# Performance work log

Measured on AMD Instinct MI355X. Metric: run time of the kernel, lower is better.

## Reference

```python
import jax, jax.numpy as jnp
import numpy as np

D_MODEL = 1024
N_HEADS = 16
HEAD_DIM = D_MODEL // N_HEADS  # 64


def setup_inputs() -> dict:
    key = jax.random.key(0)
    k1, k2, k3 = jax.random.split(key, 3)
    x = jax.random.normal(k1, (2, 2048, D_MODEL), dtype=jnp.float32)
    # nn.Linear(d, 3d, bias=False): store transposed so y = x @ W
    w_qkv = jax.random.normal(k2, (D_MODEL, 3 * D_MODEL), dtype=jnp.float32) * (D_MODEL ** -0.5)
    w_proj = jax.random.normal(k3, (D_MODEL, D_MODEL), dtype=jnp.float32) * (D_MODEL ** -0.5)
    return {"x": x, "w_qkv": w_qkv, "w_proj": w_proj}


def reference(x, w_qkv, w_proj):
    b, n, _ = x.shape
    qkv = x @ w_qkv  # [b, n, 3*d_model]
    # einops 'b n (h d qkv) -> qkv b h n d': qkv axis is innermost of the split
    qkv = qkv.reshape(b, n, N_HEADS, HEAD_DIM, 3)
    q = jnp.moveaxis(qkv[..., 0], 1, 2)  # [b, h, n, d]
    k = jnp.moveaxis(qkv[..., 1], 1, 2)
    v = jnp.moveaxis(qkv[..., 2], 1, 2)
    scale = HEAD_DIM ** -0.5
    scores = jnp.einsum('bhqd,bhkd->bhqk', q, k) * scale  # [b, h, n, n]
    causal = jnp.tril(jnp.ones((n, n), dtype=bool))
    scores = jnp.where(causal[None, None], scores, -jnp.inf)
    attn = jax.nn.softmax(scores, axis=-1)
    out = jnp.einsum('bhqk,bhkd->bhqd', attn, v)  # [b, h, n, d]
    out = jnp.moveaxis(out, 1, 2).reshape(b, n, D_MODEL)  # 'b h n d -> b n (h d)'
    return out @ w_proj
```

## Files before the change

kernel.cpp:

```cpp
#include <hip/hip_runtime.h>
#include <cstdint>
#include <cstddef>

#define D_MODEL 1024
#define N_HEADS 16
#define HEAD_DIM 64
#define SEQ 2048
#define BATCH 2

typedef __attribute__((ext_vector_type(8))) short bf16x8;
typedef __attribute__((ext_vector_type(4))) float f32x4;

__device__ inline unsigned short f2bf(float f) {
    union { float f; unsigned u; } v; v.f = f;
    unsigned r = v.u + 0x7fffu + ((v.u >> 16) & 1u);
    return (unsigned short)(r >> 16);
}

__device__ __forceinline__ unsigned cvtpk_bf16(float lo, float hi) {
    unsigned r;
    asm("v_cvt_pk_bf16_f32 %0, %1, %2" : "=v"(r) : "v"(lo), "v"(hi));
    return r;
}
__device__ __forceinline__ unsigned short f2bf_hw(float f) {
    return (unsigned short)cvtpk_bf16(f, 0.f);
}

__device__ __forceinline__ void gload_lds16(const unsigned short* g, unsigned short* l) {
    __builtin_amdgcn_global_load_lds(
        (const __attribute__((address_space(1))) unsigned int*)g,
        (__attribute__((address_space(3))) unsigned int*)l, 16, 0, 0);
}

#define WAITCNT_VM4 0x0F74
#define WAITCNT_VM0 0x0F70

__global__ __launch_bounds__(256) void fused_convert_kernel(
    const float* __restrict__ X, unsigned short* __restrict__ Xb,
    const float* __restrict__ Wq, unsigned short* __restrict__ Wqt,
    const float* __restrict__ Wp, unsigned short* __restrict__ Wpt)
{
    const int blk = blockIdx.x;
    const int tid = threadIdx.x;
    __shared__ float t[32][33];

    if (blk < 2048) {
        const int idx = blk * 256 + tid;
        const float4* src = (const float4*)X;
        float4 v0 = src[idx * 2], v1 = src[idx * 2 + 1];
        uint4 o;
        o.x = cvtpk_bf16(v0.x, v0.y);
        o.y = cvtpk_bf16(v0.z, v0.w);
        o.z = cvtpk_bf16(v1.x, v1.y);
        o.w = cvtpk_bf16(v1.z, v1.w);
        ((uint4*)Xb)[idx] = o;
    } else if (blk < 5120) {
        const int bb = blk - 2048;
        const int c0 = (bb % 96) * 32, r0 = (bb / 96) * 32;
        const int a = tid & 31, b = tid >> 5;
#pragma unroll
        for (int i = 0; i < 32; i += 8)
            t[b + i][a] = Wq[(size_t)(r0 + b + i) * (3 * D_MODEL) + c0 + a];
        __syncthreads();
#pragma unroll
        for (int i = 0; i < 32; i += 8) {
            const int c = c0 + b + i;
            const int which = c % 3;
            const int np = which * 1024 + c / 3;
            const float s = (which == 0) ? 0.125f : 1.0f;
            Wqt[(size_t)np * D_MODEL + r0 + a] = f2bf_hw(t[a][b + i] * s);
        }
    } else {
        const int bb = blk - 5120;
        const int c0 = (bb % 32) * 32, r0 = (bb / 32) * 32;
        const int a = tid & 31, b = tid >> 5;
#pragma unroll
        for (int i = 0; i < 32; i += 8)
            t[b + i][a] = Wp[(size_t)(r0 + b + i) * D_MODEL + c0 + a];
        __syncthreads();
#pragma unroll
        for (int i = 0; i < 32; i += 8)
            Wpt[(size_t)(c0 + b + i) * D_MODEL + r0 + a] = f2bf_hw(t[a][b + i]);
    }
}

#define GEMM_PIPE3_BODY(A_, B_, KBASE, NITER, BX_, BY_)                        \
    const int tid = threadIdx.x;                                               \
    const int w = tid >> 6, lane = tid & 63;                                   \
    const int l15 = lane & 15, quad = lane >> 4;                               \
    const int wr = w >> 1, wc = w & 1;                                         \
    const int row0 = (BY_) * 128, col0 = (BX_) * 128;                          \
    __shared__ unsigned short As[3][4096];                                     \
    __shared__ unsigned short Bs[3][4096];                                     \
    const f32x4 zero4 = {0.f, 0.f, 0.f, 0.f};                                  \
    f32x4 acc[4][4];                                                           \
    _Pragma("unroll") for (int i = 0; i < 4; i++)                              \
        _Pragma("unroll") for (int j = 0; j < 4; j++) acc[i][j] = zero4;       \
    auto stage_ = [&](int sb_, int kt_) {                                      \
        const int k0 = (KBASE) + kt_ * 32 + quad * 8;                          \
        _Pragma("unroll") for (int i = 0; i < 2; i++) {                        \
            const int f = w * 2 + i;                                           \
            gload_lds16((A_) + (size_t)(row0 + f * 16 + l15) * D_MODEL + k0,   \
                        &As[sb_][f * 512 + lane * 8]);                         \
            gload_lds16((B_) + (size_t)(col0 + f * 16 + l15) * D_MODEL + k0,   \
                        &Bs[sb_][f * 512 + lane * 8]);                         \
        }                                                                      \
    };                                                                         \
    stage_(0, 0);                                                              \
    stage_(1, 1);                                                              \
    int sb = 0;                                                                \
    for (int kt = 0; kt < (NITER); kt++) {                                     \
        if (kt < (NITER) - 1) {                                                \
            __builtin_amdgcn_s_waitcnt(WAITCNT_VM4);                           \
            __builtin_amdgcn_s_barrier();                                      \
            if (kt + 2 < (NITER)) stage_((sb + 2 > 2) ? sb - 1 : sb + 2, kt + 2); \
        } else {                                                               \
            __builtin_amdgcn_s_waitcnt(WAITCNT_VM0);                           \
            __builtin_amdgcn_s_barrier();                                      \
        }                                                                      \
        bf16x8 af[4], bfr[4];                                                  \
        _Pragma("unroll") for (int i = 0; i < 4; i++)                          \
            af[i] = *(const bf16x8*)&As[sb][(wr * 4 + i) * 512 + lane * 8];    \
        _Pragma("unroll") for (int j = 0; j < 4; j++)                          \
            bfr[j] = *(const bf16x8*)&Bs[sb][(wc * 4 + j) * 512 + lane * 8];   \
        __builtin_amdgcn_s_setprio(1);                                         \
        _Pragma("unroll") for (int i = 0; i < 4; i++)                          \
            _Pragma("unroll") for (int j = 0; j < 4; j++)                      \
                acc[i][j] = __builtin_amdgcn_mfma_f32_16x16x32_bf16(           \
                    af[i], bfr[j], acc[i][j], 0, 0, 0);                        \
        __builtin_amdgcn_s_setprio(0);                                         \
        sb = (sb == 2) ? 0 : sb + 1;                                           \
    }

__global__ __launch_bounds__(256) void gemm_qkv_mfma(
    const unsigned short* __restrict__ A, const unsigned short* __restrict__ B,
    unsigned short* __restrict__ Q, unsigned short* __restrict__ Kq,
    unsigned short* __restrict__ Vt)
{
    const int lin = blockIdx.x + 24 * blockIdx.y;
    const int xcd = lin & 7, t = lin >> 3;
    const int bx = (xcd & 1) * 12 + t % 12;
    const int by = (xcd >> 1) * 8 + t / 12;
    GEMM_PIPE3_BODY(A, B, 0, 32, bx, by)
    const int nbase = col0 + wc * 64;
    const int which = nbase >> 10;
    if (which < 2) {
        unsigned short* const dst = (which == 0) ? Q : Kq;
#pragma unroll
        for (int i = 0; i < 4; i++) {
            const int rowb = row0 + wr * 64 + i * 16 + quad * 4;
            const int bb = rowb >> 11, n = rowb & (SEQ - 1);
#pragma unroll
            for (int rp = 0; rp < 2; rp++) {
#pragma unroll
                for (int j = 0; j < 4; j++) {
                    const unsigned u = cvtpk_bf16(acc[i][j][2 * rp], acc[i][j][2 * rp + 1]);
                    const int idx = (nbase + j * 16 + l15) & 1023;
                    const int h = idx >> 6, dd = idx & 63;
                    unsigned short* p =
                        dst + (((size_t)(bb * N_HEADS + h)) * SEQ + n + 2 * rp) * HEAD_DIM + dd;
                    p[0] = (unsigned short)u;
                    p[HEAD_DIM] = (unsigned short)(u >> 16);
                }
            }
        }
    } else {
#pragma unroll
        for (int i = 0; i < 4; i++) {
            const int rowb = row0 + wr * 64 + i * 16 + quad * 4;
            const int bb = rowb >> 11, n = rowb & (SEQ - 1);
#pragma unroll
            for (int rp = 0; rp < 2; rp++) {
#pragma unroll
                for (int j = 0; j < 4; j++) {
                    const unsigned u = cvtpk_bf16(acc[i][j][2 * rp], acc[i][j][2 * rp + 1]);
                    const int idx = (nbase + j * 16 + l15) & 1023;
                    *(unsigned*)&Vt[((size_t)(bb * N_HEADS + (idx >> 6)) * HEAD_DIM
                                     + (idx & 63)) * SEQ + n + 2 * rp] = u;
                }
            }
        }
    }
}

__global__ __launch_bounds__(256) void gemm_proj_splitk(
    const unsigned short* __restrict__ A, const unsigned short* __restrict__ B,
    float* __restrict__ P)
{
    const int lin = blockIdx.x + 8 * blockIdx.y;
    const int xcd = lin & 7, t = lin >> 3;
    const int bx = (xcd & 1) * 4 + t % 4;
    const int by = (xcd >> 1) * 8 + t / 4;
    const int kbase = blockIdx.z * 512;
    GEMM_PIPE3_BODY(A, B, kbase, 16, bx, by)
    float* const dst = P + (size_t)blockIdx.z * (4096ull * 1024ull);
#pragma unroll
    for (int i = 0; i < 4; i++) {
#pragma unroll
        for (int r = 0; r < 4; r++) {
            const int row = row0 + wr * 64 + i * 16 + quad * 4 + r;
#pragma unroll
            for (int j = 0; j < 4; j++) {
                const int c = col0 + wc * 64 + j * 16 + l15;
                dst[(size_t)row * D_MODEL + c] = acc[i][j][r];
            }
        }
    }
}

__global__ __launch_bounds__(256) void add_out_kernel(
    const float* __restrict__ P, float* __restrict__ out)
{
    const float4* p0 = (const float4*)P;
    const float4* p1 = (const float4*)(P + 4096ull * 1024ull);
    float4* o = (float4*)out;
    const int base = (blockIdx.x * 256 + threadIdx.x) * 4;
#pragma unroll
    for (int j = 0; j < 4; j++) {
        float4 a = p0[base + j], b = p1[base + j];
        float4 r = {a.x + b.x, a.y + b.y, a.z + b.z, a.w + b.w};
        o[base + j] = r;
    }
}

__global__ __launch_bounds__(256) void flash_attn_kernel(
    const unsigned short* __restrict__ Q,
    const unsigned short* __restrict__ K,
    const unsigned short* __restrict__ Vt,
    unsigned short* __restrict__ O)
{
    const int idx = blockIdx.x;
    const int bh = idx & 31;
    const int qt2 = idx >> 5;
    const int hi = qt2 >> 3, lo = qt2 & 7;
    const int qt = (hi == 0) ? lo : (hi == 1) ? 31 - lo : (hi == 2) ? lo + 8 : 23 - lo;

    const int tid = threadIdx.x;
    const int w = tid >> 6, lane = tid & 63;
    const int l15 = lane & 15, quad = lane >> 4;

    __shared__ unsigned short Ks[2][4096];
    __shared__ unsigned short Vs[2][4096];
    __shared__ unsigned short Ps[4][1024];

    bf16x8 qf[2];
    {
        const unsigned short* qrow =
            Q + ((size_t)bh * SEQ + qt * 64 + w * 16 + l15) * HEAD_DIM;
        qf[0] = *(const bf16x8*)(qrow + quad * 8);
        qf[1] = *(const bf16x8*)(qrow + 32 + quad * 8);
    }

    const f32x4 zero4 = {0.f, 0.f, 0.f, 0.f};
    f32x4 o_acc[4] = {zero4, zero4, zero4, zero4};
    float m_i = -1e30f, l_i = 0.f;

    auto stage = [&](int bf, int kt_t) {
        const int key0 = kt_t * 64;
#pragma unroll
        for (int i = 0; i < 2; i++) {
            const int f = w * 2 + i;
            const int ct = f >> 1, kh = f & 1;
            gload_lds16(K + ((size_t)bh * SEQ + key0 + ct * 16 + l15) * HEAD_DIM
                          + kh * 32 + quad * 8,
                        &Ks[bf][f * 512 + lane * 8]);
            gload_lds16(Vt + ((size_t)bh * HEAD_DIM + ct * 16 + l15) * SEQ
                           + key0 + kh * 32 + quad * 8,
                        &Vs[bf][f * 512 + lane * 8]);
        }
    };

    stage(0, 0);
    int buf = 0;

    const int qg = qt * 64 + w * 16 + l15;

    for (int kt = 0; kt <= qt; kt++) {
        __syncthreads();
        if (kt < qt) stage(buf ^ 1, kt + 1);

        f32x4 st[4] = {zero4, zero4, zero4, zero4};
        __builtin_amdgcn_s_setprio(1);
#pragma unroll
        for (int kh = 0; kh < 2; kh++) {
#pragma unroll
            for (int ct = 0; ct < 4; ct++) {
                bf16x8 kf = *(const bf16x8*)&Ks[buf][(ct * 2 + kh) * 512 + lane * 8];
                st[ct] = __builtin_amdgcn_mfma_f32_16x16x32_bf16(kf, qf[kh], st[ct], 0, 0, 0);
            }
        }
        __builtin_amdgcn_s_setprio(0);

        float mt = -1e30f;
        if (kt == qt) {
#pragma unroll
            for (int ct = 0; ct < 4; ct++) {
#pragma unroll
                for (int r = 0; r < 4; r++) {
                    const int kg = kt * 64 + ct * 16 + quad * 4 + r;
                    float v = (kg > qg) ? -1e30f : st[ct][r];
                    st[ct][r] = v;
                    mt = fmaxf(mt, v);
                }
            }
        } else {
#pragma unroll
            for (int ct = 0; ct < 4; ct++)
#pragma unroll
                for (int r = 0; r < 4; r++)
                    mt = fmaxf(mt, st[ct][r]);
        }
        mt = fmaxf(mt, __shfl_xor(mt, 16));
        mt = fmaxf(mt, __shfl_xor(mt, 32));

        float mn = m_i;
        if (!__all(mt <= m_i + 8.0f)) {
            mn = fmaxf(m_i, mt);
            const float alpha = __expf(m_i - mn);
            m_i = mn;
            l_i *= alpha;
            float ar[4];
#pragma unroll
            for (int r = 0; r < 4; r++)
                ar[r] = __shfl(alpha, (lane & 48) | (quad * 4 + r));
#pragma unroll
            for (int dt = 0; dt < 4; dt++)
#pragma unroll
                for (int r = 0; r < 4; r++)
                    o_acc[dt][r] *= ar[r];
        }

        float ls = 0.f;
#pragma unroll
        for (int ct = 0; ct < 4; ct++) {
            const float p0 = __expf(st[ct][0] - mn);
            const float p1 = __expf(st[ct][1] - mn);
            const float p2 = __expf(st[ct][2] - mn);
            const float p3 = __expf(st[ct][3] - mn);
            ls += (p0 + p1) + (p2 + p3);
            uint2 pk2;
            pk2.x = cvtpk_bf16(p0, p1);
            pk2.y = cvtpk_bf16(p2, p3);
            const int addr = (ct >> 1) * 512 + ((ct & 1) * 2 + (quad >> 1)) * 128
                           + l15 * 8 + (quad & 1) * 4;
            *(uint2*)&Ps[w][addr] = pk2;
        }
        l_i += ls;

        __builtin_amdgcn_s_setprio(1);
#pragma unroll
        for (int kh = 0; kh < 2; kh++) {
            bf16x8 pa = *(const bf16x8*)&Ps[w][kh * 512 + quad * 128 + l15 * 8];
#pragma unroll
            for (int dt = 0; dt < 4; dt++) {
                bf16x8 vf = *(const bf16x8*)&Vs[buf][(dt * 2 + kh) * 512 + lane * 8];
                o_acc[dt] = __builtin_amdgcn_mfma_f32_16x16x32_bf16(pa, vf, o_acc[dt], 0, 0, 0);
            }
        }
        __builtin_amdgcn_s_setprio(0);
        buf ^= 1;
    }

    l_i += __shfl_xor(l_i, 16);
    l_i += __shfl_xor(l_i, 32);
    const float linv = 1.0f / l_i;
    float lr[4];
#pragma unroll
    for (int r = 0; r < 4; r++)
        lr[r] = __shfl(linv, (lane & 48) | (quad * 4 + r));

    const int b = bh >> 4, h = bh & 15;
#pragma unroll
    for (int r = 0; r < 4; r++) {
        const int q = qt * 64 + w * 16 + quad * 4 + r;
        unsigned short* orow = O + ((size_t)b * SEQ + q) * D_MODEL + h * HEAD_DIM;
#pragma unroll
        for (int dt = 0; dt < 4; dt++)
            orow[dt * 16 + l15] = f2bf_hw(o_acc[dt][r] * lr[r]);
    }
}

extern "C" void kernel_launch(void* const* d_in, const int* in_sizes, int n_in,
                              void* d_out, int out_size, void* d_ws, size_t ws_size,
                              hipStream_t stream) {
    const float* x      = (const float*)d_in[0];
    const float* w_qkv  = (const float*)d_in[1];
    const float* w_proj = (const float*)d_in[2];
    float* out = (float*)d_out;

    unsigned short* Xb  = (unsigned short*)d_ws;
    unsigned short* Wqt = Xb  + (size_t)4 * 1024 * 1024;
    unsigned short* Wpt = Wqt + (size_t)3 * 1024 * 1024;
    unsigned short* Qb  = Wpt + (size_t)1 * 1024 * 1024;
    unsigned short* Kb  = Qb  + (size_t)4 * 1024 * 1024;
    unsigned short* Vb  = Kb  + (size_t)4 * 1024 * 1024;
    unsigned short* Vtb = Vb  + (size_t)4 * 1024 * 1024;
    unsigned short* Ob  = Vtb + (size_t)4 * 1024 * 1024;

    float* Pp = (float*)Qb;

    fused_convert_kernel<<<dim3(6144), 256, 0, stream>>>(
        x, Xb, w_qkv, Wqt, w_proj, Wpt);

    gemm_qkv_mfma<<<dim3(3 * D_MODEL / 128, BATCH * SEQ / 128), 256, 0, stream>>>(
        Xb, Wqt, Qb, Kb, Vtb);

    flash_attn_kernel<<<dim3(SEQ / 64 * BATCH * N_HEADS), 256, 0, stream>>>(
        Qb, Kb, Vtb, Ob);

    gemm_proj_splitk<<<dim3(D_MODEL / 128, BATCH * SEQ / 128, 2), 256, 0, stream>>>(
        Ob, Wpt, Pp);

    add_out_kernel<<<dim3(1024), 256, 0, stream>>>(Pp, out);
}
```

Measured before the change: 212.2 us.

## Enlarge GEMM tiles to 256x128 with 8 waves and asymmetric A/B buffering

Both the QKV and projection GEMMs now use 256x128 output tiles computed by 512-thread blocks (8 waves, each owning a 128x32 sub-tile) with a K step of 64. A is triple-buffered and B double-buffered in LDS. The aim is more reuse per global load and fewer barriers per unit of K work. In exchange, LDS use per block is larger and there are half as many blocks (384 for QKV, 256 for the projection), which may hurt occupancy and load balance across CUs.

```diff
diff --git a/kernel.cpp b/kernel.cpp
--- a/kernel.cpp
+++ b/kernel.cpp
@@ -10,12 +10,6 @@
 
 typedef __attribute__((ext_vector_type(8))) short bf16x8;
 typedef __attribute__((ext_vector_type(4))) float f32x4;
-
-__device__ inline unsigned short f2bf(float f) {
-    union { float f; unsigned u; } v; v.f = f;
-    unsigned r = v.u + 0x7fffu + ((v.u >> 16) & 1u);
-    return (unsigned short)(r >> 16);
-}
 
 __device__ __forceinline__ unsigned cvtpk_bf16(float lo, float hi) {
     unsigned r;
@@ -84,81 +78,90 @@
     }
 }
 
-#define GEMM_PIPE3_BODY(A_, B_, KBASE, NITER, BX_, BY_)                        \
+#define GEMM_A3B2_BODY(A_, B_, KBASE, NITER, BX_, BY_)                         \
     const int tid = threadIdx.x;                                               \
     const int w = tid >> 6, lane = tid & 63;                                   \
     const int l15 = lane & 15, quad = lane >> 4;                               \
-    const int wr = w >> 1, wc = w & 1;                                         \
-    const int row0 = (BY_) * 128, col0 = (BX_) * 128;                          \
-    __shared__ unsigned short As[3][4096];                                     \
-    __shared__ unsigned short Bs[3][4096];                                     \
+    const int wr = w >> 2, wc = w & 3;                                         \
+    const int row0 = (BY_) * 256, col0 = (BX_) * 128;                          \
+    __shared__ unsigned short As[3 * 16384];                                   \
+    __shared__ unsigned short Bs[2 * 8192];                                    \
     const f32x4 zero4 = {0.f, 0.f, 0.f, 0.f};                                  \
-    f32x4 acc[4][4];                                                           \
-    _Pragma("unroll") for (int i = 0; i < 4; i++)                              \
-        _Pragma("unroll") for (int j = 0; j < 4; j++) acc[i][j] = zero4;       \
-    auto stage_ = [&](int sb_, int kt_) {                                      \
-        const int k0 = (KBASE) + kt_ * 32 + quad * 8;                          \
-        _Pragma("unroll") for (int i = 0; i < 2; i++) {                        \
-            const int f = w * 2 + i;                                           \
-            gload_lds16((A_) + (size_t)(row0 + f * 16 + l15) * D_MODEL + k0,   \
-                        &As[sb_][f * 512 + lane * 8]);                         \
-            gload_lds16((B_) + (size_t)(col0 + f * 16 + l15) * D_MODEL + k0,   \
-                        &Bs[sb_][f * 512 + lane * 8]);                         \
+    f32x4 acc[8][2];                                                           \
+    _Pragma("unroll") for (int i = 0; i < 8; i++)                              \
+        _Pragma("unroll") for (int j = 0; j < 2; j++) acc[i][j] = zero4;       \
+    auto stage_A = [&](int slot, int kt_) {                                    \
+        _Pragma("unroll") for (int p = 0; p < 4; p++) {                        \
+            const int fb = w * 4 + p, f = fb >> 1, kk = fb & 1;                \
+            gload_lds16((A_) + (size_t)(row0 + f * 16 + l15) * D_MODEL         \
+                            + (KBASE) + kt_ * 64 + kk * 32 + quad * 8,         \
+                        &As[slot * 16384 + fb * 512 + lane * 8]);              \
         }                                                                      \
     };                                                                         \
-    stage_(0, 0);                                                              \
-    stage_(1, 1);                                                              \
-    int sb = 0;                                                                \
-    for (int kt = 0; kt < (NITER); kt++) {                                     \
-        if (kt < (NITER) - 1) {                                                \
-            __builtin_amdgcn_s_waitcnt(WAITCNT_VM4);                           \
-            __builtin_amdgcn_s_barrier();                                      \
-            if (kt + 2 < (NITER)) stage_((sb + 2 > 2) ? sb - 1 : sb + 2, kt + 2); \
-        } else {                                                               \
-            __builtin_amdgcn_s_waitcnt(WAITCNT_VM0);                           \
-            __builtin_amdgcn_s_barrier();                                      \
+    auto stage_B = [&](int slot, int kt_) {                                    \
+        _Pragma("unroll") for (int p = 0; p < 2; p++) {                        \
+            const int fb = w * 2 + p, g = fb >> 1, kk = fb & 1;                \
+            gload_lds16((B_) + (size_t)(col0 + g * 16 + l15) * D_MODEL         \
+                            + (KBASE) + kt_ * 64 + kk * 32 + quad * 8,         \
+                        &Bs[slot * 8192 + fb * 512 + lane * 8]);               \
         }                                                                      \
-        bf16x8 af[4], bfr[4];                                                  \
-        _Pragma("unroll") for (int i = 0; i < 4; i++)                          \
-            af[i] = *(const bf16x8*)&As[sb][(wr * 4 + i) * 512 + lane * 8];    \
-        _Pragma("unroll") for (int j = 0; j < 4; j++)                          \
-            bfr[j] = *(const bf16x8*)&Bs[sb][(wc * 4 + j) * 512 + lane * 8];   \
-        __builtin_amdgcn_s_setprio(1);                                         \
-        _Pragma("unroll") for (int i = 0; i < 4; i++)                          \
-            _Pragma("unroll") for (int j = 0; j < 4; j++)                      \
-                acc[i][j] = __builtin_amdgcn_mfma_f32_16x16x32_bf16(           \
-                    af[i], bfr[j], acc[i][j], 0, 0, 0);                        \
-        __builtin_amdgcn_s_setprio(0);                                         \
-        sb = (sb == 2) ? 0 : sb + 1;                                           \
-    }
-
-__global__ __launch_bounds__(256) void gemm_qkv_mfma(
+    };                                                                         \
+    stage_B(0, 0);                                                             \
+    stage_A(0, 0);                                                             \
+    stage_A(1 % 3, 1);                                                         \
+    for (int t = 0; t < (NITER); t++) {                                        \
+        if (t < (NITER) - 1) __builtin_amdgcn_s_waitcnt(WAITCNT_VM4);          \
+        else                 __builtin_amdgcn_s_waitcnt(WAITCNT_VM0);          \
+        __builtin_amdgcn_s_barrier();                                          \
+        __builtin_amdgcn_sched_barrier(0);                                     \
+        if (t + 1 < (NITER)) stage_B((t + 1) & 1, t + 1);                      \
+        if (t + 2 < (NITER)) stage_A((t + 2) % 3, t + 2);                      \
+        const int sa = (t % 3) * 16384, sbb = (t & 1) * 8192;                  \
+        _Pragma("unroll") for (int kk = 0; kk < 2; kk++) {                     \
+            bf16x8 af[8], bfr[2];                                              \
+            _Pragma("unroll") for (int i = 0; i < 8; i++)                      \
+                af[i] = *(const bf16x8*)&As[sa + ((wr * 8 + i) * 2 + kk) * 512 \
+                                            + lane * 8];                       \
+            _Pragma("unroll") for (int j = 0; j < 2; j++)                      \
+                bfr[j] = *(const bf16x8*)&Bs[sbb + ((wc * 2 + j) * 2 + kk) * 512 \
+                                             + lane * 8];                      \
+            __builtin_amdgcn_s_setprio(1);                                     \
+            _Pragma("unroll") for (int i = 0; i < 8; i++)                      \
+                _Pragma("unroll") for (int j = 0; j < 2; j++)                  \
+                    acc[i][j] = __builtin_amdgcn_mfma_f32_16x16x32_bf16(       \
+                        af[i], bfr[j], acc[i][j], 0, 0, 0);                    \
+            __builtin_amdgcn_s_setprio(0);                                     \
+        }                                                                      \
+    }
+
+__global__ __launch_bounds__(512, 2) void gemm_qkv_mfma(
     const unsigned short* __restrict__ A, const unsigned short* __restrict__ B,
     unsigned short* __restrict__ Q, unsigned short* __restrict__ Kq,
     unsigned short* __restrict__ Vt)
 {
     const int lin = blockIdx.x + 24 * blockIdx.y;
-    const int xcd = lin & 7, t = lin >> 3;
-    const int bx = (xcd & 1) * 12 + t % 12;
-    const int by = (xcd >> 1) * 8 + t / 12;
-    GEMM_PIPE3_BODY(A, B, 0, 32, bx, by)
-    const int nbase = col0 + wc * 64;
+    const int xcd = lin & 7, tt = lin >> 3;
+    const int bx = (xcd & 1) * 12 + tt % 12;
+    const int by = (xcd >> 1) * 4 + tt / 12;
+    GEMM_A3B2_BODY(A, B, 0, 16, bx, by)
+    const int nbase = col0 + wc * 32;
     const int which = nbase >> 10;
+    const int hh = (nbase >> 6) & 15;
+    const int dbase = nbase & 63;
     if (which < 2) {
         unsigned short* const dst = (which == 0) ? Q : Kq;
 #pragma unroll
-        for (int i = 0; i < 4; i++) {
-            const int rowb = row0 + wr * 64 + i * 16 + quad * 4;
+        for (int i = 0; i < 8; i++) {
+            const int rowb = row0 + wr * 128 + i * 16 + quad * 4;
             const int bb = rowb >> 11, n = rowb & (SEQ - 1);
 #pragma unroll
             for (int rp = 0; rp < 2; rp++) {
 #pragma unroll
-                for (int j = 0; j < 4; j++) {
+                for (int j = 0; j < 2; j++) {
                     const unsigned u = cvtpk_bf16(acc[i][j][2 * rp], acc[i][j][2 * rp + 1]);
-                    const int idx = (nbase + j * 16 + l15) & 1023;
-                    const int h = idx >> 6, dd = idx & 63;
+                    const int dd = dbase + j * 16 + l15;
                     unsigned short* p =
-                        dst + (((size_t)(bb * N_HEADS + h)) * SEQ + n + 2 * rp) * HEAD_DIM + dd;
+                        dst + (((size_t)(bb * N_HEADS + hh)) * SEQ + n + 2 * rp) * HEAD_DIM + dd;
                     p[0] = (unsigned short)u;
                     p[HEAD_DIM] = (unsigned short)(u >> 16);
                 }
@@ -166,42 +169,42 @@
         }
     } else {
 #pragma unroll
-        for (int i = 0; i < 4; i++) {
-            const int rowb = row0 + wr * 64 + i * 16 + quad * 4;
+        for (int i = 0; i < 8; i++) {
+            const int rowb = row0 + wr * 128 + i * 16 + quad * 4;
             const int bb = rowb >> 11, n = rowb & (SEQ - 1);
 #pragma unroll
             for (int rp = 0; rp < 2; rp++) {
 #pragma unroll
-                for (int j = 0; j < 4; j++) {
+                for (int j = 0; j < 2; j++) {
                     const unsigned u = cvtpk_bf16(acc[i][j][2 * rp], acc[i][j][2 * rp + 1]);
-                    const int idx = (nbase + j * 16 + l15) & 1023;
-                    *(unsigned*)&Vt[((size_t)(bb * N_HEADS + (idx >> 6)) * HEAD_DIM
-                                     + (idx & 63)) * SEQ + n + 2 * rp] = u;
+                    const int dd = dbase + j * 16 + l15;
+                    *(unsigned*)&Vt[((size_t)(bb * N_HEADS + hh) * HEAD_DIM + dd) * SEQ
+                                    + n + 2 * rp] = u;
                 }
             }
         }
     }
 }
 
-__global__ __launch_bounds__(256) void gemm_proj_splitk(
+__global__ __launch_bounds__(512, 2) void gemm_proj_splitk(
     const unsigned short* __restrict__ A, const unsigned short* __restrict__ B,
     float* __restrict__ P)
 {
     const int lin = blockIdx.x + 8 * blockIdx.y;
-    const int xcd = lin & 7, t = lin >> 3;
-    const int bx = (xcd & 1) * 4 + t % 4;
-    const int by = (xcd >> 1) * 8 + t / 4;
+    const int xcd = lin & 7, tt = lin >> 3;
+    const int bx = (xcd & 1) * 4 + tt % 4;
+    const int by = (xcd >> 1) * 4 + tt / 4;
     const int kbase = blockIdx.z * 512;
-    GEMM_PIPE3_BODY(A, B, kbase, 16, bx, by)
+    GEMM_A3B2_BODY(A, B, kbase, 8, bx, by)
     float* const dst = P + (size_t)blockIdx.z * (4096ull * 1024ull);
 #pragma unroll
-    for (int i = 0; i < 4; i++) {
+    for (int i = 0; i < 8; i++) {
 #pragma unroll
         for (int r = 0; r < 4; r++) {
-            const int row = row0 + wr * 64 + i * 16 + quad * 4 + r;
-#pragma unroll
-            for (int j = 0; j < 4; j++) {
-                const int c = col0 + wc * 64 + j * 16 + l15;
+            const int row = row0 + wr * 128 + i * 16 + quad * 4 + r;
+#pragma unroll
+            for (int j = 0; j < 2; j++) {
+                const int c = col0 + wc * 32 + j * 16 + l15;
                 dst[(size_t)row * D_MODEL + c] = acc[i][j][r];
             }
         }
@@ -402,13 +405,13 @@
     fused_convert_kernel<<<dim3(6144), 256, 0, stream>>>(
         x, Xb, w_qkv, Wqt, w_proj, Wpt);
 
-    gemm_qkv_mfma<<<dim3(3 * D_MODEL / 128, BATCH * SEQ / 128), 256, 0, stream>>>(
+    gemm_qkv_mfma<<<dim3(24, 16), 512, 0, stream>>>(
         Xb, Wqt, Qb, Kb, Vtb);
 
     flash_attn_kernel<<<dim3(SEQ / 64 * BATCH * N_HEADS), 256, 0, stream>>>(
         Qb, Kb, Vtb, Ob);
 
-    gemm_proj_splitk<<<dim3(D_MODEL / 128, BATCH * SEQ / 128, 2), 256, 0, stream>>>(
+    gemm_proj_splitk<<<dim3(8, 16, 2), 512, 0, stream>>>(
         Ob, Wpt, Pp);
 
     add_out_kernel<<<dim3(1024), 256, 0, stream>>>(Pp, out);
```

Result: slower. 229.9 us (+8.3%).
